# Kernel optimization log

Hardware: AMD Instinct MI355X
Metric: run time of the kernel (lower is better)

## Reference

```python
import jax, jax.numpy as jnp
import numpy as np

N, GS, M = 128, 4, 64
C_IN, D, L = 128, 512, 8
LIN_D, OUT_DIM = 128, 1


def _gml_layer(G, h, W, b):
    # h: [N,M,C], W: [GS,P,C], b: [GS,P], G: [N,GS,M,M]
    multi = jnp.einsum('nmc,gpc->gnmp', h, W) + b[:, None, None, :]  # [GS,N,M,P]
    xo = jnp.einsum('ngij,gnjp->ngip', G, multi)                      # [N,GS,M,P]
    xo = jax.nn.relu(xo)
    return jnp.max(xo, axis=1)                                        # goodmax over GS


def setup_inputs() -> dict:
    key = jax.random.key(0)
    ks = jax.random.split(key, 12)
    s = 0.05
    return {
        'G': jax.random.uniform(ks[0], (N, GS, M, M), dtype=jnp.float32),
        'x': jax.random.normal(ks[1], (N, M, C_IN), dtype=jnp.float32),
        'W0': jax.random.normal(ks[2], (GS, D, C_IN), dtype=jnp.float32) * s,
        'b0': jax.random.normal(ks[3], (GS, D), dtype=jnp.float32) * s,
        'W': jax.random.normal(ks[4], (L - 1, GS, D, D), dtype=jnp.float32) * s,
        'b': jax.random.normal(ks[5], (L - 1, GS, D), dtype=jnp.float32) * s,
        'lin1_w': jax.random.normal(ks[6], (LIN_D, D), dtype=jnp.float32) * s,
        'lin1_b': jax.random.normal(ks[7], (LIN_D,), dtype=jnp.float32) * s,
        'lin2_w': jax.random.normal(ks[8], (OUT_DIM, LIN_D), dtype=jnp.float32) * s,
        'lin2_b': jax.random.normal(ks[9], (OUT_DIM,), dtype=jnp.float32) * s,
    }


def reference(G, x, W0, b0, W, b, lin1_w, lin1_b, lin2_w, lin2_b):
    # layer 0: C_IN -> D, shapes differ so no residual
    h = _gml_layer(G, x, W0, b0)  # [N,M,D]

    def step(h, wb):
        w, bb = wb
        return _gml_layer(G, h, w, bb) + h, None  # resnet residual (same shape)

    h, _ = jax.lax.scan(step, h, (W, b))  # L-1 layers of D -> D

    x1 = jnp.einsum('nmd,ed->nme', h, lin1_w) + lin1_b
    x2 = jnp.einsum('nme,oe->nmo', jax.nn.relu(x1), lin2_w) + lin2_b
    return x2  # [N, M, OUT_DIM]
```

## Files before the change

kernel.cpp:

```cpp
#include <hip/hip_runtime.h>

typedef float f32x4 __attribute__((ext_vector_type(4)));
typedef short s16x8 __attribute__((ext_vector_type(8)));
typedef short s16x4 __attribute__((ext_vector_type(4)));
typedef int   i32x4 __attribute__((ext_vector_type(4)));

using abfrag = s16x8;

#define DI __device__ __forceinline__

DI unsigned short f2bf(float x) {
  unsigned u = __builtin_bit_cast(unsigned, x);
  u += 0x7fffu + ((u >> 16) & 1u);
  return (unsigned short)(u >> 16);
}
DI float bf2f(unsigned short h) {
  return __builtin_bit_cast(float, ((unsigned)h) << 16);
}

DI f32x4 MFMA(abfrag a, abfrag b, f32x4 c) {
  return __builtin_amdgcn_mfma_f32_16x16x32_bf16(a, b, c, 0, 0, 0);
}

DI void gld16(void* lds_base, const void* gsrc) {
  __builtin_amdgcn_global_load_lds(
      (const __attribute__((address_space(1))) unsigned int*)gsrc,
      (__attribute__((address_space(3))) unsigned int*)lds_base, 16, 0, 0);
}

__global__ void f2bf_kernel(const float* __restrict__ src,
                            unsigned short* __restrict__ dst, int n4) {
  int i = blockIdx.x * blockDim.x + threadIdx.x;
  const int stride = gridDim.x * blockDim.x;
  for (; i < n4; i += stride) {
    f32x4 v = ((const f32x4*)src)[i];
    s16x4 o;
#pragma unroll
    for (int j = 0; j < 4; ++j) o[j] = (short)f2bf(v[j]);
    ((s16x4*)dst)[i] = o;
  }
}

template <int C, bool RES>
__global__ __launch_bounds__(256, 2) void gml_layer_kernel(
    const unsigned short* __restrict__ hin,
    const unsigned short* __restrict__ Wb,
    const float* __restrict__ bias,
    const unsigned short* __restrict__ Gb,
    unsigned short* __restrict__ hout) {
  constexpr int NT = C / 64;
  __shared__ short lds[4096 + 4 * 128 * 64];
  short* lh = lds;
  short* lw = lds + 4096;

  const int tid  = threadIdx.x;
  const int wv   = tid >> 6;
  const int lane = tid & 63;
  const int l15  = tid & 15;
  const int l7   = l15 & 7;
  const int gq   = (tid >> 4) & 3;
  const int bid  = blockIdx.x;
  const int n    = bid & 127;
  const int pc0  = (bid >> 7) * 128;

  const int lrow  = lane >> 3;
  const int lsoff = (((lane & 7) ^ lrow) << 3);

  const unsigned short* hsrc = hin + (size_t)n * 64 * C;
  const unsigned short* wsrc = Wb + (size_t)(wv * 512 + pc0) * C;
  const unsigned short* gsrc = Gb + (size_t)(n * 4 + wv) * 4096;

  float bvv[4][2];
#pragma unroll
  for (int g = 0; g < 4; ++g)
#pragma unroll
    for (int u = 0; u < 2; ++u)
      bvv[g][u] = bias[g * 512 + pc0 + 32 * wv + 16 * u + l15];

  f32x4 acc[4][4][2];
#pragma unroll
  for (int g = 0; g < 4; ++g)
#pragma unroll
    for (int t = 0; t < 4; ++t)
#pragma unroll
      for (int u = 0; u < 2; ++u)
        acc[g][t][u] = f32x4{bvv[g][u], bvv[g][u], bvv[g][u], bvv[g][u]};

  for (int kt = 0; kt < NT; ++kt) {
    const unsigned short* hkt = hsrc + kt * 64 + lsoff;
#pragma unroll
    for (int j = 0; j < 2; ++j)
      gld16(lh + (16 * wv + 8 * j) * 64, hkt + (size_t)(16 * wv + 8 * j + lrow) * C);
    const unsigned short* wkt = wsrc + kt * 64 + lsoff;
#pragma unroll
    for (int j = 0; j < 16; ++j)
      gld16(lw + (wv * 128 + 8 * j) * 64, wkt + (size_t)(8 * j + lrow) * C);
    asm volatile("s_waitcnt vmcnt(0)" ::: "memory");
    __syncthreads();

#pragma unroll
    for (int ks = 0; ks < 2; ++ks) {
      const int so = ((4 * ks + gq) ^ l7) << 3;
      abfrag a[4];
#pragma unroll
      for (int t = 0; t < 4; ++t)
        a[t] = *(const abfrag*)&lh[(16 * t + l15) * 64 + so];
#pragma unroll
      for (int g = 0; g < 4; ++g) {
#pragma unroll
        for (int u = 0; u < 2; ++u) {
          abfrag b = *(const abfrag*)&lw[(g * 128 + 32 * wv + 16 * u + l15) * 64 + so];
#pragma unroll
          for (int t = 0; t < 4; ++t) acc[g][t][u] = MFMA(a[t], b, acc[g][t][u]);
        }
      }
    }
    __syncthreads();
  }

#pragma unroll
  for (int j = 0; j < 8; ++j)
    gld16(lw + (wv * 64 + 8 * j) * 64, gsrc + (8 * j + lrow) * 64 + lsoff);
  asm volatile("s_waitcnt vmcnt(0)" ::: "memory");
  __syncthreads();

  f32x4 xmax[4][2];
#pragma unroll
  for (int t = 0; t < 4; ++t)
#pragma unroll
    for (int u = 0; u < 2; ++u) xmax[t][u] = f32x4{0.f, 0.f, 0.f, 0.f};

#pragma unroll
  for (int g = 0; g < 4; ++g) {
    abfrag bb[2][2];
#pragma unroll
    for (int s = 0; s < 2; ++s)
#pragma unroll
      for (int u = 0; u < 2; ++u) {
        abfrag t8;
#pragma unroll
        for (int r = 0; r < 4; ++r) {
          t8[r]     = (short)f2bf(acc[g][s][u][r]);
          t8[4 + r] = (short)f2bf(acc[g][s + 2][u][r]);
        }
        bb[s][u] = t8;
      }
    f32x4 xg[4][2];
#pragma unroll
    for (int t = 0; t < 4; ++t)
#pragma unroll
      for (int u = 0; u < 2; ++u) xg[t][u] = f32x4{0.f, 0.f, 0.f, 0.f};
#pragma unroll
    for (int t = 0; t < 4; ++t) {
      const short* grow = lw + (g * 64 + 16 * t + l15) * 64;
#pragma unroll
      for (int s = 0; s < 2; ++s) {
        const int slot = 2 * s + (gq >> 1);
        const int e1 = ((slot ^ l7) << 3) + ((gq & 1) << 2);
        const int e2 = (((slot + 4) ^ l7) << 3) + ((gq & 1) << 2);
        s16x4 alo = *(const s16x4*)(grow + e1);
        s16x4 ahi = *(const s16x4*)(grow + e2);
        abfrag a;
#pragma unroll
        for (int j = 0; j < 4; ++j) { a[j] = alo[j]; a[4 + j] = ahi[j]; }
#pragma unroll
        for (int u = 0; u < 2; ++u) xg[t][u] = MFMA(a, bb[s][u], xg[t][u]);
      }
    }
#pragma unroll
    for (int t = 0; t < 4; ++t)
#pragma unroll
      for (int u = 0; u < 2; ++u)
#pragma unroll
        for (int r = 0; r < 4; ++r)
          xmax[t][u][r] = fmaxf(xmax[t][u][r], xg[t][u][r]);
  }

#pragma unroll
  for (int t = 0; t < 4; ++t)
#pragma unroll
    for (int u = 0; u < 2; ++u)
#pragma unroll
      for (int r = 0; r < 4; ++r) {
        const int m = 16 * t + 4 * gq + r;
        const int d = pc0 + 32 * wv + 16 * u + l15;
        float v = xmax[t][u][r];
        if constexpr (RES) v += bf2f(hin[(size_t)(n * 64 + m) * C + d]);
        hout[(size_t)(n * 64 + m) * 512 + d] = f2bf(v);
      }
}

__global__ __launch_bounds__(256, 2) void final_kernel(
    const unsigned short* __restrict__ hin,
    const float* __restrict__ w1,
    const float* __restrict__ b1,
    const float* __restrict__ w2,
    const float* __restrict__ b2,
    float* __restrict__ out) {
  constexpr int KT = 64, LW = 72, C = 512, NT = C / KT;
  __shared__ short sh_h[2][64][LW];
  __shared__ short sh_w[2][128][LW];
  __shared__ float red[4][64];
  const int tid = threadIdx.x;
  const int wv  = tid >> 6;
  const int l15 = tid & 15;
  const int gq  = (tid >> 4) & 3;
  const int n   = blockIdx.x;
  const int srow = tid >> 3;
  const int scol = (tid & 7) * 8;
  const unsigned short* hsrc = hin + (size_t)n * 64 * C;

  f32x4 acc[4][2];
#pragma unroll
  for (int t = 0; t < 4; ++t)
#pragma unroll
    for (int u = 0; u < 2; ++u) acc[t][u] = f32x4{0.f, 0.f, 0.f, 0.f};

  i32x4 hr[2], wr[4];
#pragma unroll
  for (int p = 0; p < 2; ++p)
    hr[p] = *(const i32x4*)(hsrc + (srow + p * 32) * C + scol);
#pragma unroll
  for (int p = 0; p < 4; ++p) {
    const float* s = w1 + (srow + p * 32) * C + scol;
    f32x4 v0 = *(const f32x4*)s;
    f32x4 v1 = *(const f32x4*)(s + 4);
    s16x8 o;
#pragma unroll
    for (int j = 0; j < 4; ++j) { o[j] = (short)f2bf(v0[j]); o[4 + j] = (short)f2bf(v1[j]); }
    wr[p] = __builtin_bit_cast(i32x4, o);
  }
#pragma unroll
  for (int p = 0; p < 2; ++p) *(i32x4*)&sh_h[0][srow + p * 32][scol] = hr[p];
#pragma unroll
  for (int p = 0; p < 4; ++p) *(i32x4*)&sh_w[0][srow + p * 32][scol] = wr[p];

  for (int kt = 0; kt < NT; ++kt) {
    const int cur = kt & 1;
    if (kt + 1 < NT) {
#pragma unroll
      for (int p = 0; p < 2; ++p)
        hr[p] = *(const i32x4*)(hsrc + (srow + p * 32) * C + (kt + 1) * KT + scol);
#pragma unroll
      for (int p = 0; p < 4; ++p) {
        const float* s = w1 + (srow + p * 32) * C + (kt + 1) * KT + scol;
        f32x4 v0 = *(const f32x4*)s;
        f32x4 v1 = *(const f32x4*)(s + 4);
        s16x8 o;
#pragma unroll
        for (int j = 0; j < 4; ++j) { o[j] = (short)f2bf(v0[j]); o[4 + j] = (short)f2bf(v1[j]); }
        wr[p] = __builtin_bit_cast(i32x4, o);
      }
    }
    __syncthreads();
#pragma unroll
    for (int ks = 0; ks < 2; ++ks) {
      abfrag a[4], b[2];
#pragma unroll
      for (int t = 0; t < 4; ++t)
        a[t] = *(const abfrag*)&sh_h[cur][16 * t + l15][ks * 32 + gq * 8];
#pragma unroll
      for (int u = 0; u < 2; ++u)
        b[u] = *(const abfrag*)&sh_w[cur][32 * wv + 16 * u + l15][ks * 32 + gq * 8];
#pragma unroll
      for (int t = 0; t < 4; ++t)
#pragma unroll
        for (int u = 0; u < 2; ++u) acc[t][u] = MFMA(a[t], b[u], acc[t][u]);
    }
    if (kt + 1 < NT) {
#pragma unroll
      for (int p = 0; p < 2; ++p) *(i32x4*)&sh_h[1 - cur][srow + p * 32][scol] = hr[p];
#pragma unroll
      for (int p = 0; p < 4; ++p) *(i32x4*)&sh_w[1 - cur][srow + p * 32][scol] = wr[p];
    }
  }

  float b1v[2], w2v[2];
#pragma unroll
  for (int u = 0; u < 2; ++u) {
    b1v[u] = b1[32 * wv + 16 * u + l15];
    w2v[u] = w2[32 * wv + 16 * u + l15];
  }
  float part[4][4];
#pragma unroll
  for (int t = 0; t < 4; ++t)
#pragma unroll
    for (int r = 0; r < 4; ++r) {
      float s0 = 0.f;
#pragma unroll
      for (int u = 0; u < 2; ++u)
        s0 += fmaxf(acc[t][u][r] + b1v[u], 0.f) * w2v[u];
      part[t][r] = s0;
    }
#pragma unroll
  for (int t = 0; t < 4; ++t)
#pragma unroll
    for (int r = 0; r < 4; ++r)
#pragma unroll
      for (int msk = 1; msk < 16; msk <<= 1)
        part[t][r] += __shfl_xor(part[t][r], msk);
  if (l15 == 0) {
#pragma unroll
    for (int t = 0; t < 4; ++t)
#pragma unroll
      for (int r = 0; r < 4; ++r) red[wv][16 * t + 4 * gq + r] = part[t][r];
  }
  __syncthreads();
  if (tid < 64)
    out[(size_t)n * 64 + tid] =
        red[0][tid] + red[1][tid] + red[2][tid] + red[3][tid] + b2[0];
}

extern "C" void kernel_launch(void* const* d_in, const int* in_sizes, int n_in,
                              void* d_out, int out_size, void* d_ws, size_t ws_size,
                              hipStream_t stream) {
  const float* G   = (const float*)d_in[0];
  const float* x   = (const float*)d_in[1];
  const float* W0  = (const float*)d_in[2];
  const float* b0  = (const float*)d_in[3];
  const float* W   = (const float*)d_in[4];
  const float* b   = (const float*)d_in[5];
  const float* l1w = (const float*)d_in[6];
  const float* l1b = (const float*)d_in[7];
  const float* l2w = (const float*)d_in[8];
  const float* l2b = (const float*)d_in[9];
  float* out = (float*)d_out;

  char* p = (char*)d_ws;
  unsigned short* W0b = (unsigned short*)p; p += (size_t)4 * 512 * 128 * 2;
  unsigned short* Wb  = (unsigned short*)p; p += (size_t)7 * 4 * 512 * 512 * 2;
  unsigned short* Gb  = (unsigned short*)p; p += (size_t)128 * 4 * 64 * 64 * 2;
  unsigned short* xb  = (unsigned short*)p; p += (size_t)128 * 64 * 128 * 2;
  unsigned short* hA  = (unsigned short*)p; p += (size_t)128 * 64 * 512 * 2;
  unsigned short* hB  = (unsigned short*)p; p += (size_t)128 * 64 * 512 * 2;

  auto cvt = [&](const float* s, unsigned short* d, long long nel) {
    int n4 = (int)(nel / 4);
    int blocks = (n4 + 255) / 256;
    if (blocks > 4096) blocks = 4096;
    f2bf_kernel<<<blocks, 256, 0, stream>>>(s, d, n4);
  };
  cvt(W0, W0b, 4LL * 512 * 128);
  cvt(W,  Wb,  7LL * 4 * 512 * 512);
  cvt(G,  Gb,  128LL * 4 * 64 * 64);
  cvt(x,  xb,  128LL * 64 * 128);

  gml_layer_kernel<128, false><<<512, 256, 0, stream>>>(xb, W0b, b0, Gb, hA);
  const unsigned short* src = hA;
  unsigned short* dst = hB;
  for (int i = 0; i < 7; ++i) {
    gml_layer_kernel<512, true><<<512, 256, 0, stream>>>(
        src, Wb + (size_t)i * 4 * 512 * 512, b + (size_t)i * 4 * 512, Gb, dst);
    const unsigned short* t = src; src = dst; dst = (unsigned short*)t;
  }
  final_kernel<<<128, 256, 0, stream>>>(src, l1w, l1b, l2w, l2b, out);
}
```

Baseline: 188.1 us.

## Stream W fragments directly into registers and double-buffer h tiles in LDS

The layer kernel now loads weight B-fragments straight from global memory into registers and prefetches them one k-slice ahead, so the large W tile no longer goes through LDS. The h tile is double-buffered in LDS with register prefetch, which leaves one barrier per k-step instead of two. The G tile load is issued at kernel start into its own LDS buffer so it overlaps the first GEMM. The four fp32-to-bf16 conversion launches are merged into one multi-source kernel that writes a contiguous workspace. The trade-off is more register pressure and uncoalesced-per-wave global loads for W, which leans on cache reuse across blocks.

Result: slower. 323.2 us (+71.8%).

```diff
diff --git a/kernel.cpp b/kernel.cpp
--- a/kernel.cpp
+++ b/kernel.cpp
@@ -28,12 +28,21 @@
       (__attribute__((address_space(3))) unsigned int*)lds_base, 16, 0, 0);
 }
 
-__global__ void f2bf_kernel(const float* __restrict__ src,
-                            unsigned short* __restrict__ dst, int n4) {
+__global__ void f2bf_multi(const float* __restrict__ s0, int n0,
+                           const float* __restrict__ s1, int n1,
+                           const float* __restrict__ s2, int n2,
+                           const float* __restrict__ s3, int n3,
+                           unsigned short* __restrict__ dst) {
+  const int total = n0 + n1 + n2 + n3;
   int i = blockIdx.x * blockDim.x + threadIdx.x;
   const int stride = gridDim.x * blockDim.x;
-  for (; i < n4; i += stride) {
-    f32x4 v = ((const f32x4*)src)[i];
+  for (; i < total; i += stride) {
+    const float* s; int off;
+    if (i < n0) { s = s0; off = i; }
+    else if (i < n0 + n1) { s = s1; off = i - n0; }
+    else if (i < n0 + n1 + n2) { s = s2; off = i - n0 - n1; }
+    else { s = s3; off = i - n0 - n1 - n2; }
+    f32x4 v = ((const f32x4*)s)[off];
     s16x4 o;
 #pragma unroll
     for (int j = 0; j < 4; ++j) o[j] = (short)f2bf(v[j]);
@@ -49,9 +58,8 @@
     const unsigned short* __restrict__ Gb,
     unsigned short* __restrict__ hout) {
   constexpr int NT = C / 64;
-  __shared__ short lds[4096 + 4 * 128 * 64];
-  short* lh = lds;
-  short* lw = lds + 4096;
+  __shared__ short lh[2][64][64];
+  __shared__ short lg[4][64][64];
 
   const int tid  = threadIdx.x;
   const int wv   = tid >> 6;
@@ -59,68 +67,104 @@
   const int l15  = tid & 15;
   const int l7   = l15 & 7;
   const int gq   = (tid >> 4) & 3;
-  const int bid  = blockIdx.x;
-  const int n    = bid & 127;
-  const int pc0  = (bid >> 7) * 128;
-
-  const int lrow  = lane >> 3;
-  const int lsoff = (((lane & 7) ^ lrow) << 3);
+  const int n    = blockIdx.x & 127;
+  const int pc0  = (blockIdx.x >> 7) * 128;
+  const int lrow = lane >> 3;
+  const int s8   = lane & 7;
+  const int lsoff = ((s8 ^ lrow) << 3);
 
   const unsigned short* hsrc = hin + (size_t)n * 64 * C;
-  const unsigned short* wsrc = Wb + (size_t)(wv * 512 + pc0) * C;
   const unsigned short* gsrc = Gb + (size_t)(n * 4 + wv) * 4096;
 
-  float bvv[4][2];
+#pragma unroll
+  for (int j = 0; j < 8; ++j)
+    gld16(&lg[wv][8 * j][0], gsrc + (8 * j + lrow) * 64 + lsoff);
+
+  const unsigned short* wgu[4][2];
 #pragma unroll
   for (int g = 0; g < 4; ++g)
 #pragma unroll
     for (int u = 0; u < 2; ++u)
-      bvv[g][u] = bias[g * 512 + pc0 + 32 * wv + 16 * u + l15];
+      wgu[g][u] = Wb + (size_t)(g * 512 + pc0 + 16 * u) * C;
+  const int loff = (32 * wv + l15) * C + gq * 8;
 
   f32x4 acc[4][4][2];
 #pragma unroll
   for (int g = 0; g < 4; ++g)
 #pragma unroll
-    for (int t = 0; t < 4; ++t)
+    for (int u = 0; u < 2; ++u) {
+      const float bv = bias[g * 512 + pc0 + 32 * wv + 16 * u + l15];
+#pragma unroll
+      for (int t = 0; t < 4; ++t) acc[g][t][u] = f32x4{bv, bv, bv, bv};
+    }
+
+  const int hrow0 = 16 * wv + lrow;
+  {
+    i32x4 h0 = *(const i32x4*)(hsrc + (size_t)hrow0 * C + s8 * 8);
+    i32x4 h1 = *(const i32x4*)(hsrc + (size_t)(hrow0 + 8) * C + s8 * 8);
+    *(i32x4*)&lh[0][hrow0][lsoff] = h0;
+    *(i32x4*)&lh[0][hrow0 + 8][lsoff] = h1;
+  }
+
+  i32x4 bcur[8], bnxt[8];
+  auto loadB = [&](i32x4* d, int kt, int ks) {
+#pragma unroll
+    for (int g = 0; g < 4; ++g)
 #pragma unroll
       for (int u = 0; u < 2; ++u)
-        acc[g][t][u] = f32x4{bvv[g][u], bvv[g][u], bvv[g][u], bvv[g][u]};
+        d[g * 2 + u] = *(const i32x4*)(wgu[g][u] + loff + kt * 64 + ks * 32);
+  };
+  loadB(bcur, 0, 0);
+  asm volatile("s_waitcnt lgkmcnt(0)" ::: "memory");
 
   for (int kt = 0; kt < NT; ++kt) {
-    const unsigned short* hkt = hsrc + kt * 64 + lsoff;
-#pragma unroll
-    for (int j = 0; j < 2; ++j)
-      gld16(lh + (16 * wv + 8 * j) * 64, hkt + (size_t)(16 * wv + 8 * j + lrow) * C);
-    const unsigned short* wkt = wsrc + kt * 64 + lsoff;
-#pragma unroll
-    for (int j = 0; j < 16; ++j)
-      gld16(lw + (wv * 128 + 8 * j) * 64, wkt + (size_t)(8 * j + lrow) * C);
-    asm volatile("s_waitcnt vmcnt(0)" ::: "memory");
-    __syncthreads();
-
-#pragma unroll
-    for (int ks = 0; ks < 2; ++ks) {
-      const int so = ((4 * ks + gq) ^ l7) << 3;
+    const int cur = kt & 1;
+    i32x4 hA, hB;
+    if (kt + 1 < NT) {
+      hA = *(const i32x4*)(hsrc + (size_t)hrow0 * C + (kt + 1) * 64 + s8 * 8);
+      hB = *(const i32x4*)(hsrc + (size_t)(hrow0 + 8) * C + (kt + 1) * 64 + s8 * 8);
+    }
+    asm volatile("" ::: "memory");
+    __builtin_amdgcn_s_barrier();
+    asm volatile("" ::: "memory");
+
+    loadB(bnxt, kt, 1);
+    {
       abfrag a[4];
 #pragma unroll
       for (int t = 0; t < 4; ++t)
-        a[t] = *(const abfrag*)&lh[(16 * t + l15) * 64 + so];
-#pragma unroll
-      for (int g = 0; g < 4; ++g) {
+        a[t] = *(const abfrag*)&lh[cur][16 * t + l15][(gq ^ l7) << 3];
+#pragma unroll
+      for (int g = 0; g < 4; ++g)
 #pragma unroll
         for (int u = 0; u < 2; ++u) {
-          abfrag b = *(const abfrag*)&lw[(g * 128 + 32 * wv + 16 * u + l15) * 64 + so];
+          const abfrag b = __builtin_bit_cast(abfrag, bcur[g * 2 + u]);
 #pragma unroll
           for (int t = 0; t < 4; ++t) acc[g][t][u] = MFMA(a[t], b, acc[g][t][u]);
         }
-      }
-    }
-    __syncthreads();
-  }
-
-#pragma unroll
-  for (int j = 0; j < 8; ++j)
-    gld16(lw + (wv * 64 + 8 * j) * 64, gsrc + (8 * j + lrow) * 64 + lsoff);
+    }
+    if (kt + 1 < NT) loadB(bcur, kt + 1, 0);
+    {
+      abfrag a[4];
+#pragma unroll
+      for (int t = 0; t < 4; ++t)
+        a[t] = *(const abfrag*)&lh[cur][16 * t + l15][((4 + gq) ^ l7) << 3];
+#pragma unroll
+      for (int g = 0; g < 4; ++g)
+#pragma unroll
+        for (int u = 0; u < 2; ++u) {
+          const abfrag b = __builtin_bit_cast(abfrag, bnxt[g * 2 + u]);
+#pragma unroll
+          for (int t = 0; t < 4; ++t) acc[g][t][u] = MFMA(a[t], b, acc[g][t][u]);
+        }
+    }
+    if (kt + 1 < NT) {
+      *(i32x4*)&lh[1 - cur][hrow0][lsoff] = hA;
+      *(i32x4*)&lh[1 - cur][hrow0 + 8][lsoff] = hB;
+      asm volatile("s_waitcnt lgkmcnt(0)" ::: "memory");
+    }
+  }
+
   asm volatile("s_waitcnt vmcnt(0)" ::: "memory");
   __syncthreads();
 
@@ -152,7 +196,7 @@
       for (int u = 0; u < 2; ++u) xg[t][u] = f32x4{0.f, 0.f, 0.f, 0.f};
 #pragma unroll
     for (int t = 0; t < 4; ++t) {
-      const short* grow = lw + (g * 64 + 16 * t + l15) * 64;
+      const short* grow = &lg[g][16 * t + l15][0];
 #pragma unroll
       for (int s = 0; s < 2; ++s) {
         const int slot = 2 * s + (gq >> 1);
@@ -334,16 +378,11 @@
   unsigned short* hA  = (unsigned short*)p; p += (size_t)128 * 64 * 512 * 2;
   unsigned short* hB  = (unsigned short*)p; p += (size_t)128 * 64 * 512 * 2;
 
-  auto cvt = [&](const float* s, unsigned short* d, long long nel) {
-    int n4 = (int)(nel / 4);
-    int blocks = (n4 + 255) / 256;
-    if (blocks > 4096) blocks = 4096;
-    f2bf_kernel<<<blocks, 256, 0, stream>>>(s, d, n4);
-  };
-  cvt(W0, W0b, 4LL * 512 * 128);
-  cvt(W,  Wb,  7LL * 4 * 512 * 512);
-  cvt(G,  Gb,  128LL * 4 * 64 * 64);
-  cvt(x,  xb,  128LL * 64 * 128);
+  const int n0 = 4 * 512 * 128 / 4;
+  const int n1 = 7 * 4 * 512 * 512 / 4;
+  const int n2 = 128 * 4 * 64 * 64 / 4;
+  const int n3 = 128 * 64 * 128 / 4;
+  f2bf_multi<<<2048, 256, 0, stream>>>(W0, n0, W, n1, G, n2, x, n3, W0b);
 
   gml_layer_kernel<128, false><<<512, 256, 0, stream>>>(xb, W0b, b0, Gb, hA);
   const unsigned short* src = hA;
```
